# Optimization experiments

Measured on AMD Instinct MI355X. Metric: run time of the kernel, lower is better.

## Reference

```python
import jax, jax.numpy as jnp
import numpy as np
import math

B, L, DIN, DOUT = 4, 1024, 64, 10
D, N = 512, 16            # hidden_dim (d_model), state_dim (d_state)
R = math.ceil(D / 16)     # dt_rank = 32
DT_MIN, DT_MAX = 1e-3, 1e-1


def _mamba_params(key):
    k1, k2, k3 = jax.random.split(key, 3)
    xproj_w = jax.random.normal(k1, (R + 2 * N, D), jnp.float32) * (D ** -0.5)
    dt_std = R ** -0.5
    dtproj_w = jax.random.uniform(k2, (D, R), jnp.float32, -dt_std, dt_std)
    dt = jnp.exp(jax.random.uniform(k3, (D,), jnp.float32)
                 * (math.log(DT_MAX) - math.log(DT_MIN)) + math.log(DT_MIN))
    dt = jnp.clip(dt, 1e-4, None)
    dtproj_b = dt + jnp.log(-jnp.expm1(-dt))          # inverse softplus
    A_log = jnp.log(jnp.broadcast_to(jnp.arange(1, N + 1, dtype=jnp.float32), (D, N)))
    Dp = jnp.ones((D,), jnp.float32)
    return xproj_w, dtproj_w, dtproj_b, A_log, Dp


def setup_inputs() -> dict:
    key = jax.random.key(0)
    ks = jax.random.split(key, 8)
    inp = {
        'x': jax.random.normal(ks[0], (B, L, DIN), jnp.float32),
        'W_in': jax.random.normal(ks[1], (D, DIN), jnp.float32) * (DIN ** -0.5),
        'b_in': jnp.zeros((D,), jnp.float32),
        'mix1_w': jax.random.normal(ks[2], (D, D), jnp.float32) * (D ** -0.5),
        'mix1_b': jnp.zeros((D,), jnp.float32),
        'mix2_w': jax.random.normal(ks[3], (D, D), jnp.float32) * (D ** -0.5),
        'mix2_b': jnp.zeros((D,), jnp.float32),
        'out_w': jax.random.normal(ks[4], (DOUT, D), jnp.float32) * (D ** -0.5),
        'out_b': jnp.zeros((DOUT,), jnp.float32),
    }
    (inp['m1_xproj'], inp['m1_dtw'], inp['m1_dtb'], inp['m1_Alog'], inp['m1_D']) = _mamba_params(ks[5])
    (inp['m2_xproj'], inp['m2_dtw'], inp['m2_dtb'], inp['m2_Alog'], inp['m2_D']) = _mamba_params(ks[6])
    return inp


def mamba_block(h, xproj_w, dtproj_w, dtproj_b, A_log, Dp):
    # h: (b, l, d) ; selective scan with A = -exp(A_log), delta_softplus=True
    b, l, d = h.shape
    A = -jnp.exp(A_log)                              # (d, n)
    x_dbl = jnp.einsum('bld,rd->blr', h, xproj_w)    # (b, l, r+2n)
    dt, Bm, Cm = jnp.split(x_dbl, [R, R + N], axis=-1)
    delta = jax.nn.softplus(jnp.einsum('blr,dr->bld', dt, dtproj_w) + dtproj_b)  # (b,l,d)
    dA = jnp.exp(delta[..., None] * A)                               # (b,l,d,n)
    dBu = delta[..., None] * Bm[:, :, None, :] * h[..., None]        # (b,l,d,n)

    def step(hstate, inp_t):
        dA_t, dBu_t, C_t = inp_t                     # (b,d,n),(b,d,n),(b,n)
        hstate = dA_t * hstate + dBu_t
        y = jnp.einsum('bdn,bn->bd', hstate, C_t)
        return hstate, y

    h0 = jnp.zeros((b, d, N), h.dtype)
    _, ys = jax.lax.scan(step, h0,
                         (jnp.swapaxes(dA, 0, 1), jnp.swapaxes(dBu, 0, 1), jnp.swapaxes(Cm, 0, 1)))
    y = jnp.swapaxes(ys, 0, 1) + h * Dp              # (b, l, d)
    return y


def reference(x, W_in, b_in, m1_xproj, m1_dtw, m1_dtb, m1_Alog, m1_D,
              mix1_w, mix1_b, m2_xproj, m2_dtw, m2_dtb, m2_Alog, m2_D,
              mix2_w, mix2_b, out_w, out_b):
    h = jnp.einsum('bli,di->bld', x, W_in) + b_in
    y = h
    h = mamba_block(h, m1_xproj, m1_dtw, m1_dtb, m1_Alog, m1_D)
    h = jax.nn.gelu(h, approximate=False)
    h = jnp.einsum('bld,ed->ble', h, mix1_w) + mix1_b
    h = h + y
    y = h
    h = mamba_block(h, m2_xproj, m2_dtw, m2_dtb, m2_Alog, m2_D)
    h = jax.nn.gelu(h, approximate=False)
    h = jnp.einsum('bld,ed->ble', h, mix2_w) + mix2_b
    h = h + y
    h = h.mean(axis=1)                               # (b, d)
    return jnp.einsum('bd,od->bo', h, out_w) + out_b
```

## Files before the change

kernel.cpp:

```cpp
#include <hip/hip_runtime.h>
#include <math.h>

typedef unsigned short ushort_t;
typedef short bf8_t __attribute__((ext_vector_type(8)));
typedef float f4_t  __attribute__((ext_vector_type(4)));

constexpr int B_   = 4;
constexpr int L_   = 1024;
constexpr int DIN_ = 64;
constexpr int DOUT_= 10;
constexpr int D_   = 512;
constexpr int N_   = 16;
constexpr int R_   = 32;
constexpr int RN_  = 64;
constexpr int M_   = B_ * L_;

constexpr int CN_ = 64;
constexpr int CL_ = L_ / CN_;

__device__ float    g_h   [M_ * D_];
__device__ float    g_h2  [M_ * D_];
__device__ ushort_t g_hbf [M_ * D_];
__device__ ushort_t g_gelubf[M_ * D_];
__device__ float    g_xdbl[M_ * RN_];
__device__ float    g_stL  [B_ * CN_ * D_ * N_];
__device__ float    g_sumd [B_ * CN_ * D_];
__device__ float    g_carry[B_ * CN_ * D_ * N_];
__device__ float    g_mean [B_ * D_];
__device__ ushort_t g_w1bf [D_ * D_];
__device__ ushort_t g_w2bf [D_ * D_];
__device__ ushort_t g_xp1bf[RN_ * D_];
__device__ ushort_t g_xp2bf[RN_ * D_];

__device__ __forceinline__ float gelu_f(float x) {
  return 0.5f * x * (1.0f + erff(x * 0.7071067811865475f));
}
__device__ __forceinline__ float softplus_f(float x) {
  return fmaxf(x, 0.0f) + log1pf(__expf(-fabsf(x)));
}
__device__ __forceinline__ ushort_t f2bf(float x) {
  union { float f; unsigned u; } v; v.f = x;
  unsigned r = v.u + 0x7fffu + ((v.u >> 16) & 1u);
  return (ushort_t)(r >> 16);
}

__device__ __forceinline__ void in_mfma_part(int bx,
                                             const float* __restrict__ x,
                                             const float* __restrict__ w,
                                             const float* __restrict__ bias) {
  __shared__ ushort_t As[64][72];
  __shared__ ushort_t Bs[64][72];
  const int tid  = threadIdx.x;
  const int m0   = (bx >> 3) * 64;
  const int n0   = (bx & 7) * 64;
  const int lane = tid & 63;
  const int wv   = tid >> 6;
  const int quad = lane >> 4;
  const int ln   = lane & 15;
  const int mw   = (wv & 1) * 32;
  const int nw   = (wv >> 1) * 32;

  {
    const int m = tid >> 2, q = (tid & 3) << 4;
#pragma unroll
    for (int i = 0; i < 4; ++i) {
      float4 va = *(const float4*)&x[(size_t)(m0 + m) * 64 + q + i * 4];
      float4 vb = *(const float4*)&w[(size_t)(n0 + m) * 64 + q + i * 4];
      ushort4 oa, ob;
      oa.x = f2bf(va.x); oa.y = f2bf(va.y); oa.z = f2bf(va.z); oa.w = f2bf(va.w);
      ob.x = f2bf(vb.x); ob.y = f2bf(vb.y); ob.z = f2bf(vb.z); ob.w = f2bf(vb.w);
      *(ushort4*)&As[m][q + i * 4] = oa;
      *(ushort4*)&Bs[m][q + i * 4] = ob;
    }
  }
  __syncthreads();

  f4_t acc[2][2] = {};
#pragma unroll
  for (int k1 = 0; k1 < 64; k1 += 32) {
    bf8_t a0 = *(const bf8_t*)&As[mw +      ln][k1 + quad * 8];
    bf8_t a1 = *(const bf8_t*)&As[mw + 16 + ln][k1 + quad * 8];
    bf8_t b0 = *(const bf8_t*)&Bs[nw +      ln][k1 + quad * 8];
    bf8_t b1 = *(const bf8_t*)&Bs[nw + 16 + ln][k1 + quad * 8];
    acc[0][0] = __builtin_amdgcn_mfma_f32_16x16x32_bf16(a0, b0, acc[0][0], 0, 0, 0);
    acc[0][1] = __builtin_amdgcn_mfma_f32_16x16x32_bf16(a0, b1, acc[0][1], 0, 0, 0);
    acc[1][0] = __builtin_amdgcn_mfma_f32_16x16x32_bf16(a1, b0, acc[1][0], 0, 0, 0);
    acc[1][1] = __builtin_amdgcn_mfma_f32_16x16x32_bf16(a1, b1, acc[1][1], 0, 0, 0);
  }

  float bj[2] = { bias[n0 + nw + ln], bias[n0 + nw + 16 + ln] };
#pragma unroll
  for (int i = 0; i < 2; ++i)
#pragma unroll
    for (int j = 0; j < 2; ++j) {
      const int nc = n0 + nw + 16 * j + ln;
#pragma unroll
      for (int r = 0; r < 4; ++r) {
        const int row = m0 + mw + 16 * i + quad * 4 + r;
        const size_t idx = (size_t)row * D_ + nc;
        float v = acc[i][j][r] + bj[j];
        g_h[idx] = v;
        g_hbf[idx] = f2bf(v);
      }
    }
}

__global__ __launch_bounds__(256) void k_pre(const float* __restrict__ x,
                                             const float* __restrict__ w_in,
                                             const float* __restrict__ b_in,
                                             const float* __restrict__ w1,
                                             const float* __restrict__ w2,
                                             const float* __restrict__ xp1,
                                             const float* __restrict__ xp2) {
  const int bx = blockIdx.x;
  if (bx < 512) { in_mfma_part(bx, x, w_in, b_in); return; }
  if (bx == 1088) {
#pragma unroll
    for (int j = 0; j < 8; ++j) g_mean[threadIdx.x * 8 + j] = 0.0f;
    return;
  }
  int i = ((bx - 512) * 256 + threadIdx.x) * 4;
  const float* src; ushort_t* dst; int off;
  if (i < 262144)      { src = w1;  dst = g_w1bf;  off = i; }
  else if (i < 524288) { src = w2;  dst = g_w2bf;  off = i - 262144; }
  else if (i < 557056) { src = xp1; dst = g_xp1bf; off = i - 524288; }
  else                 { src = xp2; dst = g_xp2bf; off = i - 557056; }
  float4 v = *(const float4*)&src[off];
  ushort4 o; o.x = f2bf(v.x); o.y = f2bf(v.y); o.z = f2bf(v.z); o.w = f2bf(v.w);
  *(ushort4*)&dst[off] = o;
}

template<int NN, int EPIM, bool DUAL, bool MEAN>
__device__ __forceinline__ void gemm_bf16_dev(
    const ushort_t* __restrict__ Abf, const ushort_t* __restrict__ Wbf,
    const float* __restrict__ bias, const float* __restrict__ res,
    float* __restrict__ out, ushort_t* __restrict__ obf) {
  __shared__ ushort_t As[64][72];
  __shared__ ushort_t Bs[64][72];
  constexpr int NB = NN / 64;
  const int tid  = threadIdx.x;
  const int m0   = (blockIdx.x / NB) * 64;
  const int n0   = (blockIdx.x % NB) * 64;
  const int lane = tid & 63;
  const int wv   = tid >> 6;
  const int quad = lane >> 4;
  const int ln   = lane & 15;
  const int mw   = (wv & 1) * 32;
  const int nw   = (wv >> 1) * 32;

  f4_t acc[2][2] = {};

  for (int k0 = 0; k0 < 512; k0 += 64) {
#pragma unroll
    for (int c = 0; c < 2; ++c) {
      int idx = tid + c * 256;
      int m = idx >> 3, kq = (idx & 7) << 3;
      *(float4*)&As[m][kq] = *(const float4*)&Abf[(size_t)(m0 + m) * 512 + k0 + kq];
      *(float4*)&Bs[m][kq] = *(const float4*)&Wbf[(size_t)(n0 + m) * 512 + k0 + kq];
    }
    __syncthreads();
#pragma unroll
    for (int k1 = 0; k1 < 64; k1 += 32) {
      bf8_t a0 = *(const bf8_t*)&As[mw +      ln][k1 + quad * 8];
      bf8_t a1 = *(const bf8_t*)&As[mw + 16 + ln][k1 + quad * 8];
      bf8_t b0 = *(const bf8_t*)&Bs[nw +      ln][k1 + quad * 8];
      bf8_t b1 = *(const bf8_t*)&Bs[nw + 16 + ln][k1 + quad * 8];
      acc[0][0] = __builtin_amdgcn_mfma_f32_16x16x32_bf16(a0, b0, acc[0][0], 0, 0, 0);
      acc[0][1] = __builtin_amdgcn_mfma_f32_16x16x32_bf16(a0, b1, acc[0][1], 0, 0, 0);
      acc[1][0] = __builtin_amdgcn_mfma_f32_16x16x32_bf16(a1, b0, acc[1][0], 0, 0, 0);
      acc[1][1] = __builtin_amdgcn_mfma_f32_16x16x32_bf16(a1, b1, acc[1][1], 0, 0, 0);
    }
    __syncthreads();
  }

  float bj[2] = {0.f, 0.f};
  if constexpr (EPIM == 1) {
    bj[0] = bias[n0 + nw + ln];
    bj[1] = bias[n0 + nw + 16 + ln];
  }
  float psum[2][2] = {{0.f, 0.f}, {0.f, 0.f}};
#pragma unroll
  for (int i = 0; i < 2; ++i)
#pragma unroll
    for (int j = 0; j < 2; ++j) {
      const int nc = n0 + nw + 16 * j + ln;
#pragma unroll
      for (int r = 0; r < 4; ++r) {
        const int row = m0 + mw + 16 * i + quad * 4 + r;
        const size_t idx = (size_t)row * NN + nc;
        float v = acc[i][j][r];
        if constexpr (EPIM == 1) v += bj[j] + res[idx];
        out[idx] = v;
        if constexpr (DUAL) obf[idx] = f2bf(v);
        if constexpr (MEAN) psum[i][j] += v;
      }
    }
  if constexpr (MEAN) {
    __shared__ float ssum[16][64];
#pragma unroll
    for (int i = 0; i < 2; ++i)
#pragma unroll
      for (int j = 0; j < 2; ++j) {
        const int rg = (wv & 1) * 8 + i * 4 + quad;
        const int cl = (wv >> 1) * 32 + j * 16 + ln;
        ssum[rg][cl] = psum[i][j];
      }
    __syncthreads();
    if (tid < 64) {
      float s = 0.f;
#pragma unroll
      for (int rg = 0; rg < 16; ++rg) s += ssum[rg][tid];
      const int b = m0 >> 10;
      atomicAdd(&g_mean[b * D_ + n0 + tid], s);
    }
  }
}

__global__ __launch_bounds__(256) void k_xdbl1g() {
  gemm_bf16_dev<64, 0, false, false>(g_hbf, g_xp1bf, nullptr, nullptr, g_xdbl, nullptr);
}
__global__ __launch_bounds__(256) void k_xdbl2g() {
  gemm_bf16_dev<64, 0, false, false>(g_hbf, g_xp2bf, nullptr, nullptr, g_xdbl, nullptr);
}
__global__ __launch_bounds__(256) void k_mix1g(const float* __restrict__ bias) {
  gemm_bf16_dev<512, 1, true, false>(g_gelubf, g_w1bf, bias, g_h, g_h2, g_hbf);
}
__global__ __launch_bounds__(256) void k_mix2g(const float* __restrict__ bias) {
  gemm_bf16_dev<512, 1, false, true>(g_gelubf, g_w2bf, bias, g_h2, g_h, nullptr);
}

__device__ __forceinline__ void load_A(const float* __restrict__ Alog, int d,
                                       float* A) {
#pragma unroll
  for (int n = 0; n < 16; n += 4) {
    float4 t = *(const float4*)&Alog[d * N_ + n];
    A[n + 0] = -__expf(t.x); A[n + 1] = -__expf(t.y);
    A[n + 2] = -__expf(t.z); A[n + 3] = -__expf(t.w);
  }
}

__device__ __forceinline__ void scan_p1_dev(const float* __restrict__ h,
                                            const float* __restrict__ dtw,
                                            const float* __restrict__ dtb,
                                            const float* __restrict__ Alog) {
  __shared__ float sdt[CL_][33];
  __shared__ float sB [CL_][16];
  const int d = threadIdx.x;
  const int c = blockIdx.x & (CN_ - 1);
  const int b = blockIdx.x / CN_;
  const int row0 = b * L_ + c * CL_;

  { int l = d >> 5, k = d & 31; sdt[l][k] = g_xdbl[(size_t)(row0 + l) * RN_ + k]; }
  if (d < CL_ * 16) {
    int l = d >> 4, n = d & 15;
    sB[l][n] = g_xdbl[(size_t)(row0 + l) * RN_ + R_ + n];
  }
  float w[32];
#pragma unroll
  for (int r = 0; r < 32; r += 4) {
    float4 t = *(const float4*)&dtw[d * R_ + r];
    w[r] = t.x; w[r + 1] = t.y; w[r + 2] = t.z; w[r + 3] = t.w;
  }
  const float bias = dtb[d];
  float A[16];
  load_A(Alog, d, A);
  __syncthreads();

  float st[16] = {};
  float sumd = 0.0f;
#pragma unroll
  for (int l = 0; l < CL_; ++l) {
    float acc = bias;
#pragma unroll
    for (int k = 0; k < 32; ++k) acc = fmaf(sdt[l][k], w[k], acc);
    const float delta = softplus_f(acc);
    const float dh = delta * h[(size_t)(row0 + l) * D_ + d];
    sumd += delta;
#pragma unroll
    for (int n = 0; n < 16; ++n) {
      float dA = __expf(delta * A[n]);
      st[n] = fmaf(dA, st[n], dh * sB[l][n]);
    }
  }
  const size_t o = ((size_t)(b * CN_ + c) * D_ + d) * N_;
#pragma unroll
  for (int n = 0; n < 16; n += 4)
    *(float4*)&g_stL[o + n] = make_float4(st[n], st[n+1], st[n+2], st[n+3]);
  g_sumd[(b * CN_ + c) * D_ + d] = sumd;
}

__global__ __launch_bounds__(512) void k_p1_1(const float* dtw, const float* dtb,
                                              const float* Alog) {
  scan_p1_dev(g_h, dtw, dtb, Alog);
}
__global__ __launch_bounds__(512) void k_p1_2(const float* dtw, const float* dtb,
                                              const float* Alog) {
  scan_p1_dev(g_h2, dtw, dtb, Alog);
}

__global__ __launch_bounds__(256) void k_scan_carry(const float* __restrict__ Alog) {
  const int g = blockIdx.x * 256 + threadIdx.x;
  const int n = g & 15;
  const int d = (g >> 4) & (D_ - 1);
  const int b = g >> 13;
  const float A = -__expf(Alog[d * N_ + n]);
  float carry = 0.0f;
#pragma unroll
  for (int c0 = 0; c0 < CN_; c0 += 16) {
    float s[16], p[16];
#pragma unroll
    for (int j = 0; j < 16; ++j) {
      s[j] = g_stL[((size_t)(b * CN_ + c0 + j) * D_ + d) * N_ + n];
      p[j] = g_sumd[(b * CN_ + c0 + j) * D_ + d];
    }
#pragma unroll
    for (int j = 0; j < 16; ++j) {
      g_carry[((size_t)(b * CN_ + c0 + j) * D_ + d) * N_ + n] = carry;
      carry = fmaf(__expf(A * p[j]), carry, s[j]);
    }
  }
}

__device__ __forceinline__ void scan_p2_dev(const float* __restrict__ h,
                                            const float* __restrict__ dtw,
                                            const float* __restrict__ dtb,
                                            const float* __restrict__ Alog,
                                            const float* __restrict__ Dp,
                                            ushort_t* __restrict__ ybf) {
  __shared__ float sdt[CL_][33];
  __shared__ float sBC[CL_][32];
  const int d = threadIdx.x;
  const int c = blockIdx.x & (CN_ - 1);
  const int b = blockIdx.x / CN_;
  const int row0 = b * L_ + c * CL_;

  { int l = d >> 5, k = d & 31; sdt[l][k] = g_xdbl[(size_t)(row0 + l) * RN_ + k]; }
  { int l = d >> 5, k = d & 31; sBC[l][k] = g_xdbl[(size_t)(row0 + l) * RN_ + R_ + k]; }
  float w[32];
#pragma unroll
  for (int r = 0; r < 32; r += 4) {
    float4 t = *(const float4*)&dtw[d * R_ + r];
    w[r] = t.x; w[r + 1] = t.y; w[r + 2] = t.z; w[r + 3] = t.w;
  }
  const float bias = dtb[d];
  float A[16];
  load_A(Alog, d, A);
  const float Dpv = Dp[d];
  __syncthreads();

  float st[16];
  const size_t o = ((size_t)(b * CN_ + c) * D_ + d) * N_;
#pragma unroll
  for (int n = 0; n < 16; n += 4) {
    float4 t = *(const float4*)&g_carry[o + n];
    st[n] = t.x; st[n+1] = t.y; st[n+2] = t.z; st[n+3] = t.w;
  }
#pragma unroll
  for (int l = 0; l < CL_; ++l) {
    float acc = bias;
#pragma unroll
    for (int k = 0; k < 32; ++k) acc = fmaf(sdt[l][k], w[k], acc);
    const float delta = softplus_f(acc);
    const float hv = h[(size_t)(row0 + l) * D_ + d];
    const float dh = delta * hv;
    float y = 0.0f;
#pragma unroll
    for (int n = 0; n < 16; ++n) {
      float dA = __expf(delta * A[n]);
      st[n] = fmaf(dA, st[n], dh * sBC[l][n]);
      y = fmaf(st[n], sBC[l][16 + n], y);
    }
    ybf[(size_t)(row0 + l) * D_ + d] = f2bf(gelu_f(y + hv * Dpv));
  }
}

__global__ __launch_bounds__(512) void k_p2_1(const float* dtw, const float* dtb,
                                              const float* Alog, const float* Dp) {
  scan_p2_dev(g_h, dtw, dtb, Alog, Dp, g_gelubf);
}
__global__ __launch_bounds__(512) void k_p2_2(const float* dtw, const float* dtb,
                                              const float* Alog, const float* Dp) {
  scan_p2_dev(g_h2, dtw, dtb, Alog, Dp, g_gelubf);
}

__global__ __launch_bounds__(512) void k_finalB(const float* out_w, const float* out_b,
                                                float* out) {
  __shared__ float sm[D_];
  __shared__ float sp[DOUT_ * 16];
  const int b = blockIdx.x, tid = threadIdx.x;
  sm[tid] = g_mean[b * D_ + tid] * (1.0f / L_);
  __syncthreads();
  if (tid < DOUT_ * 16) {
    int o = tid >> 4, seg = tid & 15;
    float p = 0.0f;
#pragma unroll
    for (int i = 0; i < 32; ++i)
      p += sm[seg * 32 + i] * out_w[o * D_ + seg * 32 + i];
    sp[tid] = p;
  }
  __syncthreads();
  if (tid < DOUT_) {
    float v = out_b[tid];
#pragma unroll
    for (int i = 0; i < 16; ++i) v += sp[tid * 16 + i];
    out[b * DOUT_ + tid] = v;
  }
}

extern "C" void kernel_launch(void* const* d_in, const int* in_sizes, int n_in,
                              void* d_out, int out_size, void* d_ws, size_t ws_size,
                              hipStream_t stream) {
  const float* x        = (const float*)d_in[0];
  const float* W_in     = (const float*)d_in[1];
  const float* b_in     = (const float*)d_in[2];
  const float* mix1_w   = (const float*)d_in[3];
  const float* mix1_b   = (const float*)d_in[4];
  const float* mix2_w   = (const float*)d_in[5];
  const float* mix2_b   = (const float*)d_in[6];
  const float* out_w    = (const float*)d_in[7];
  const float* out_b    = (const float*)d_in[8];
  const float* m1_xproj = (const float*)d_in[9];
  const float* m1_dtw   = (const float*)d_in[10];
  const float* m1_dtb   = (const float*)d_in[11];
  const float* m1_Alog  = (const float*)d_in[12];
  const float* m1_D     = (const float*)d_in[13];
  const float* m2_xproj = (const float*)d_in[14];
  const float* m2_dtw   = (const float*)d_in[15];
  const float* m2_dtb   = (const float*)d_in[16];
  const float* m2_Alog  = (const float*)d_in[17];
  const float* m2_D     = (const float*)d_in[18];
  float* out = (float*)d_out;

  const int gScan  = B_ * CN_;
  const int gCarry = (B_ * D_ * N_) / 256;
  const int gMix   = (M_ / 64) * (D_ / 64);
  const int gXdbl  = (M_ / 64);

  k_pre<<<1089, 256, 0, stream>>>(x, W_in, b_in, mix1_w, mix2_w, m1_xproj, m2_xproj);

  k_xdbl1g    <<<gXdbl,  256, 0, stream>>>();
  k_p1_1      <<<gScan,  512, 0, stream>>>(m1_dtw, m1_dtb, m1_Alog);
  k_scan_carry<<<gCarry, 256, 0, stream>>>(m1_Alog);
  k_p2_1      <<<gScan,  512, 0, stream>>>(m1_dtw, m1_dtb, m1_Alog, m1_D);
  k_mix1g     <<<gMix,   256, 0, stream>>>(mix1_b);
  k_xdbl2g    <<<gXdbl,  256, 0, stream>>>();
  k_p1_2      <<<gScan,  512, 0, stream>>>(m2_dtw, m2_dtb, m2_Alog);
  k_scan_carry<<<gCarry, 256, 0, stream>>>(m2_Alog);
  k_p2_2      <<<gScan,  512, 0, stream>>>(m2_dtw, m2_dtb, m2_Alog, m2_D);
  k_mix2g     <<<gMix,   256, 0, stream>>>(mix2_b);
  k_finalB<<<B_, 512, 0, stream>>>(out_w, out_b, out);
}
```

Before: 240.7 us.

## Fuse x_proj GEMM and carry scan into scan phase-1, fold final head into mix2

Scan phase 1 now computes its chunk's x_dbl rows itself with MFMA from the bf16 h and xproj tiles staged in shared memory. It also writes x_dbl out for phase 2. The last block per batch, found through an atomic counter, then runs the cross-chunk carry scan vectorised over all 16 states. The output projection is folded into the mix2 GEMM's last-finishing block the same way. This drops five kernel launches and their global round trips. The cost is a large shared-memory footprint per block, serialised tail work in a single block, and correctness that relies on threadfence and counter ordering.

```diff
diff --git a/kernel.cpp b/kernel.cpp
--- a/kernel.cpp
+++ b/kernel.cpp
@@ -27,6 +27,8 @@
 __device__ float    g_sumd [B_ * CN_ * D_];
 __device__ float    g_carry[B_ * CN_ * D_ * N_];
 __device__ float    g_mean [B_ * D_];
+__device__ int      g_cntc [8];
+__device__ int      g_cntm;
 __device__ ushort_t g_w1bf [D_ * D_];
 __device__ ushort_t g_w2bf [D_ * D_];
 __device__ ushort_t g_xp1bf[RN_ * D_];
@@ -117,6 +119,8 @@
   if (bx == 1088) {
 #pragma unroll
     for (int j = 0; j < 8; ++j) g_mean[threadIdx.x * 8 + j] = 0.0f;
+    if (threadIdx.x < 8) g_cntc[threadIdx.x] = 0;
+    if (threadIdx.x == 8) g_cntm = 0;
     return;
   }
   int i = ((bx - 512) * 256 + threadIdx.x) * 4;
@@ -216,17 +220,47 @@
   }
 }
 
-__global__ __launch_bounds__(256) void k_xdbl1g() {
-  gemm_bf16_dev<64, 0, false, false>(g_hbf, g_xp1bf, nullptr, nullptr, g_xdbl, nullptr);
-}
-__global__ __launch_bounds__(256) void k_xdbl2g() {
-  gemm_bf16_dev<64, 0, false, false>(g_hbf, g_xp2bf, nullptr, nullptr, g_xdbl, nullptr);
-}
 __global__ __launch_bounds__(256) void k_mix1g(const float* __restrict__ bias) {
   gemm_bf16_dev<512, 1, true, false>(g_gelubf, g_w1bf, bias, g_h, g_h2, g_hbf);
 }
-__global__ __launch_bounds__(256) void k_mix2g(const float* __restrict__ bias) {
+
+__global__ __launch_bounds__(256) void k_mix2g(const float* __restrict__ bias,
+                                               const float* __restrict__ out_w,
+                                               const float* __restrict__ out_b,
+                                               float* __restrict__ outp) {
   gemm_bf16_dev<512, 1, false, true>(g_gelubf, g_w2bf, bias, g_h2, g_h, nullptr);
+
+  __threadfence();
+  __shared__ int lastm;
+  if (threadIdx.x == 0) lastm = (atomicAdd(&g_cntm, 1) == 511) ? 1 : 0;
+  __syncthreads();
+  if (!lastm) return;
+  __threadfence();
+
+  const int tid = threadIdx.x;
+  __shared__ float smean[4][D_];
+  __shared__ float sp[4][DOUT_][16];
+  for (int i = tid; i < B_ * D_; i += 256)
+    smean[i >> 9][i & 511] = g_mean[i] * (1.0f / L_);
+  __syncthreads();
+#pragma unroll
+  for (int b = 0; b < B_; ++b)
+    if (tid < DOUT_ * 16) {
+      int o = tid >> 4, seg = tid & 15;
+      float p = 0.0f;
+#pragma unroll
+      for (int i = 0; i < 32; ++i)
+        p += smean[b][seg * 32 + i] * out_w[o * D_ + seg * 32 + i];
+      sp[b][o][seg] = p;
+    }
+  __syncthreads();
+  if (tid < B_ * DOUT_) {
+    int b = tid / DOUT_, o = tid % DOUT_;
+    float v = out_b[o];
+#pragma unroll
+    for (int j = 0; j < 16; ++j) v += sp[b][o][j];
+    outp[b * DOUT_ + o] = v;
+  }
 }
 
 __device__ __forceinline__ void load_A(const float* __restrict__ Alog, int d,
@@ -239,22 +273,38 @@
   }
 }
 
-__device__ __forceinline__ void scan_p1_dev(const float* __restrict__ h,
-                                            const float* __restrict__ dtw,
-                                            const float* __restrict__ dtb,
-                                            const float* __restrict__ Alog) {
-  __shared__ float sdt[CL_][33];
-  __shared__ float sB [CL_][16];
-  const int d = threadIdx.x;
-  const int c = blockIdx.x & (CN_ - 1);
-  const int b = blockIdx.x / CN_;
+__device__ __forceinline__ void p1f_dev(const float* __restrict__ h,
+                                        const ushort_t* __restrict__ hbf,
+                                        const ushort_t* __restrict__ xpbf,
+                                        const float* __restrict__ dtw,
+                                        const float* __restrict__ dtb,
+                                        const float* __restrict__ Alog,
+                                        int* __restrict__ cnt4) {
+  __shared__ ushort_t As[16][520];
+  __shared__ ushort_t Bs[64][520];
+  __shared__ float    sx[16][65];
+  const int tid  = threadIdx.x;
+  const int c    = blockIdx.x & (CN_ - 1);
+  const int b    = blockIdx.x >> 6;
   const int row0 = b * L_ + c * CL_;
-
-  { int l = d >> 5, k = d & 31; sdt[l][k] = g_xdbl[(size_t)(row0 + l) * RN_ + k]; }
-  if (d < CL_ * 16) {
-    int l = d >> 4, n = d & 15;
-    sB[l][n] = g_xdbl[(size_t)(row0 + l) * RN_ + R_ + n];
-  }
+  const int lane = tid & 63;
+  const int wv   = tid >> 6;
+  const int quad = lane >> 4;
+  const int ln   = lane & 15;
+
+#pragma unroll
+  for (int i = 0; i < 2; ++i) {
+    int idx = tid + i * 512;
+    int m = idx >> 6, kq = (idx & 63) << 3;
+    *(float4*)&As[m][kq] = *(const float4*)&hbf[(size_t)(row0 + m) * 512 + kq];
+  }
+#pragma unroll
+  for (int i = 0; i < 8; ++i) {
+    int idx = tid + i * 512;
+    int m = idx >> 6, kq = (idx & 63) << 3;
+    *(float4*)&Bs[m][kq] = *(const float4*)&xpbf[(size_t)m * 512 + kq];
+  }
+  const int d = tid;
   float w[32];
 #pragma unroll
   for (int r = 0; r < 32; r += 4) {
@@ -266,59 +316,89 @@
   load_A(Alog, d, A);
   __syncthreads();
 
+  if (wv < 4) {
+    f4_t acc = {};
+#pragma unroll
+    for (int k0 = 0; k0 < 512; k0 += 32) {
+      bf8_t a  = *(const bf8_t*)&As[ln][k0 + quad * 8];
+      bf8_t bb = *(const bf8_t*)&Bs[wv * 16 + ln][k0 + quad * 8];
+      acc = __builtin_amdgcn_mfma_f32_16x16x32_bf16(a, bb, acc, 0, 0, 0);
+    }
+#pragma unroll
+    for (int r = 0; r < 4; ++r) {
+      const int rr = quad * 4 + r, ccol = wv * 16 + ln;
+      sx[rr][ccol] = acc[r];
+      g_xdbl[(size_t)(row0 + rr) * RN_ + ccol] = acc[r];
+    }
+  }
+  __syncthreads();
+
   float st[16] = {};
   float sumd = 0.0f;
 #pragma unroll
   for (int l = 0; l < CL_; ++l) {
-    float acc = bias;
-#pragma unroll
-    for (int k = 0; k < 32; ++k) acc = fmaf(sdt[l][k], w[k], acc);
-    const float delta = softplus_f(acc);
+    float acc2 = bias;
+#pragma unroll
+    for (int k = 0; k < 32; ++k) acc2 = fmaf(sx[l][k], w[k], acc2);
+    const float delta = softplus_f(acc2);
     const float dh = delta * h[(size_t)(row0 + l) * D_ + d];
     sumd += delta;
 #pragma unroll
     for (int n = 0; n < 16; ++n) {
       float dA = __expf(delta * A[n]);
-      st[n] = fmaf(dA, st[n], dh * sB[l][n]);
-    }
-  }
-  const size_t o = ((size_t)(b * CN_ + c) * D_ + d) * N_;
-#pragma unroll
-  for (int n = 0; n < 16; n += 4)
-    *(float4*)&g_stL[o + n] = make_float4(st[n], st[n+1], st[n+2], st[n+3]);
-  g_sumd[(b * CN_ + c) * D_ + d] = sumd;
-}
-
-__global__ __launch_bounds__(512) void k_p1_1(const float* dtw, const float* dtb,
-                                              const float* Alog) {
-  scan_p1_dev(g_h, dtw, dtb, Alog);
-}
-__global__ __launch_bounds__(512) void k_p1_2(const float* dtw, const float* dtb,
-                                              const float* Alog) {
-  scan_p1_dev(g_h2, dtw, dtb, Alog);
-}
-
-__global__ __launch_bounds__(256) void k_scan_carry(const float* __restrict__ Alog) {
-  const int g = blockIdx.x * 256 + threadIdx.x;
-  const int n = g & 15;
-  const int d = (g >> 4) & (D_ - 1);
-  const int b = g >> 13;
-  const float A = -__expf(Alog[d * N_ + n]);
-  float carry = 0.0f;
-#pragma unroll
-  for (int c0 = 0; c0 < CN_; c0 += 16) {
-    float s[16], p[16];
-#pragma unroll
-    for (int j = 0; j < 16; ++j) {
-      s[j] = g_stL[((size_t)(b * CN_ + c0 + j) * D_ + d) * N_ + n];
-      p[j] = g_sumd[(b * CN_ + c0 + j) * D_ + d];
-    }
-#pragma unroll
-    for (int j = 0; j < 16; ++j) {
-      g_carry[((size_t)(b * CN_ + c0 + j) * D_ + d) * N_ + n] = carry;
-      carry = fmaf(__expf(A * p[j]), carry, s[j]);
-    }
-  }
+      st[n] = fmaf(dA, st[n], dh * sx[l][32 + n]);
+    }
+  }
+  {
+    const size_t o = ((size_t)(b * CN_ + c) * D_ + d) * N_;
+#pragma unroll
+    for (int n = 0; n < 16; n += 4)
+      *(float4*)&g_stL[o + n] = make_float4(st[n], st[n+1], st[n+2], st[n+3]);
+    g_sumd[(b * CN_ + c) * D_ + d] = sumd;
+  }
+
+  __threadfence();
+  __shared__ int lastf;
+  if (tid == 0) lastf = (atomicAdd(&cnt4[b], 1) == CN_ - 1) ? 1 : 0;
+  __syncthreads();
+  if (!lastf) return;
+  __threadfence();
+
+  float carry[16] = {};
+#pragma unroll
+  for (int c0 = 0; c0 < CN_; c0 += 8) {
+    float4 sv[8][4]; float pv[8];
+#pragma unroll
+    for (int j = 0; j < 8; ++j) {
+      const size_t base = ((size_t)(b * CN_ + c0 + j) * D_ + d) * N_;
+      sv[j][0] = *(const float4*)&g_stL[base + 0];
+      sv[j][1] = *(const float4*)&g_stL[base + 4];
+      sv[j][2] = *(const float4*)&g_stL[base + 8];
+      sv[j][3] = *(const float4*)&g_stL[base + 12];
+      pv[j] = g_sumd[(b * CN_ + c0 + j) * D_ + d];
+    }
+#pragma unroll
+    for (int j = 0; j < 8; ++j) {
+      const size_t base = ((size_t)(b * CN_ + c0 + j) * D_ + d) * N_;
+      *(float4*)&g_carry[base + 0]  = make_float4(carry[0],  carry[1],  carry[2],  carry[3]);
+      *(float4*)&g_carry[base + 4]  = make_float4(carry[4],  carry[5],  carry[6],  carry[7]);
+      *(float4*)&g_carry[base + 8]  = make_float4(carry[8],  carry[9],  carry[10], carry[11]);
+      *(float4*)&g_carry[base + 12] = make_float4(carry[12], carry[13], carry[14], carry[15]);
+      const float* sj = (const float*)&sv[j][0];
+#pragma unroll
+      for (int n = 0; n < 16; ++n)
+        carry[n] = fmaf(__expf(A[n] * pv[j]), carry[n], sj[n]);
+    }
+  }
+}
+
+__global__ __launch_bounds__(512, 2) void k_p1f_1(const float* dtw, const float* dtb,
+                                                  const float* Alog) {
+  p1f_dev(g_h, g_hbf, g_xp1bf, dtw, dtb, Alog, &g_cntc[0]);
+}
+__global__ __launch_bounds__(512, 2) void k_p1f_2(const float* dtw, const float* dtb,
+                                                  const float* Alog) {
+  p1f_dev(g_h2, g_hbf, g_xp2bf, dtw, dtb, Alog, &g_cntc[4]);
 }
 
 __device__ __forceinline__ void scan_p2_dev(const float* __restrict__ h,
@@ -381,30 +461,6 @@
 __global__ __launch_bounds__(512) void k_p2_2(const float* dtw, const float* dtb,
                                               const float* Alog, const float* Dp) {
   scan_p2_dev(g_h2, dtw, dtb, Alog, Dp, g_gelubf);
-}
-
-__global__ __launch_bounds__(512) void k_finalB(const float* out_w, const float* out_b,
-                                                float* out) {
-  __shared__ float sm[D_];
-  __shared__ float sp[DOUT_ * 16];
-  const int b = blockIdx.x, tid = threadIdx.x;
-  sm[tid] = g_mean[b * D_ + tid] * (1.0f / L_);
-  __syncthreads();
-  if (tid < DOUT_ * 16) {
-    int o = tid >> 4, seg = tid & 15;
-    float p = 0.0f;
-#pragma unroll
-    for (int i = 0; i < 32; ++i)
-      p += sm[seg * 32 + i] * out_w[o * D_ + seg * 32 + i];
-    sp[tid] = p;
-  }
-  __syncthreads();
-  if (tid < DOUT_) {
-    float v = out_b[tid];
-#pragma unroll
-    for (int i = 0; i < 16; ++i) v += sp[tid * 16 + i];
-    out[b * DOUT_ + tid] = v;
-  }
 }
 
 extern "C" void kernel_launch(void* const* d_in, const int* in_sizes, int n_in,
@@ -431,22 +487,15 @@
   const float* m2_D     = (const float*)d_in[18];
   float* out = (float*)d_out;
 
-  const int gScan  = B_ * CN_;
-  const int gCarry = (B_ * D_ * N_) / 256;
-  const int gMix   = (M_ / 64) * (D_ / 64);
-  const int gXdbl  = (M_ / 64);
+  const int gScan = B_ * CN_;
+  const int gMix  = (M_ / 64) * (D_ / 64);
 
   k_pre<<<1089, 256, 0, stream>>>(x, W_in, b_in, mix1_w, mix2_w, m1_xproj, m2_xproj);
 
-  k_xdbl1g    <<<gXdbl,  256, 0, stream>>>();
-  k_p1_1      <<<gScan,  512, 0, stream>>>(m1_dtw, m1_dtb, m1_Alog);
-  k_scan_carry<<<gCarry, 256, 0, stream>>>(m1_Alog);
-  k_p2_1      <<<gScan,  512, 0, stream>>>(m1_dtw, m1_dtb, m1_Alog, m1_D);
-  k_mix1g     <<<gMix,   256, 0, stream>>>(mix1_b);
-  k_xdbl2g    <<<gXdbl,  256, 0, stream>>>();
-  k_p1_2      <<<gScan,  512, 0, stream>>>(m2_dtw, m2_dtb, m2_Alog);
-  k_scan_carry<<<gCarry, 256, 0, stream>>>(m2_Alog);
-  k_p2_2      <<<gScan,  512, 0, stream>>>(m2_dtw, m2_dtb, m2_Alog, m2_D);
-  k_mix2g     <<<gMix,   256, 0, stream>>>(mix2_b);
-  k_finalB<<<B_, 512, 0, stream>>>(out_w, out_b, out);
-}
+  k_p1f_1<<<gScan, 512, 0, stream>>>(m1_dtw, m1_dtb, m1_Alog);
+  k_p2_1 <<<gScan, 512, 0, stream>>>(m1_dtw, m1_dtb, m1_Alog, m1_D);
+  k_mix1g<<<gMix,  256, 0, stream>>>(mix1_b);
+  k_p1f_2<<<gScan, 512, 0, stream>>>(m2_dtw, m2_dtb, m2_Alog);
+  k_p2_2 <<<gScan, 512, 0, stream>>>(m2_dtw, m2_dtb, m2_Alog, m2_D);
+  k_mix2g<<<gMix,  256, 0, stream>>>(mix2_b, out_w, out_b, out);
+}
```

After: 606.0 us. 2.52x slower.
